# Performance work log

Measured on AMD Instinct MI355X. Metric: run time of the kernel, lower is better.

## Reference

```python
import jax, jax.numpy as jnp
import numpy as np

N_NODES = 50000
N_REL = 4
N_EDGES = 400000
IN_F, HID_F, OUT_F = 128, 128, 64


def _graphconv(h, s, d, W, b, n_nodes):
    """DGL GraphConv, norm='both': D_dst^{-1/2} A D_src^{-1/2} h W + b.
    Degrees clamped to min 1 (DGL behavior for isolated nodes)."""
    ones = jnp.ones(s.shape[0], h.dtype)
    deg_out = jnp.clip(jax.ops.segment_sum(ones, s, num_segments=n_nodes), 1.0)
    deg_in = jnp.clip(jax.ops.segment_sum(ones, d, num_segments=n_nodes), 1.0)
    # scale src features, transform first (weight applied pre-aggregation)
    hw = (h * jax.lax.rsqrt(deg_out)[:, None]) @ W          # [N, out]
    msg = hw[s]                                              # gather  [E, out]
    agg = jax.ops.segment_sum(msg, d, num_segments=n_nodes)  # scatter [N, out]
    return agg * jax.lax.rsqrt(deg_in)[:, None] + b


def _hetero_layer(h, src, dst, W, b):
    # HeteroGraphConv with aggregate='sum': sum per-relation GraphConv outputs
    n_nodes = h.shape[0]
    out = _graphconv(h, src[0], dst[0], W[0], b[0], n_nodes)
    for r in range(1, W.shape[0]):
        out = out + _graphconv(h, src[r], dst[r], W[r], b[r], n_nodes)
    return out


def setup_inputs() -> dict:
    key = jax.random.key(0)
    k = jax.random.split(key, 6)
    x = jax.random.normal(k[0], (N_NODES, IN_F), dtype=jnp.float32)
    src = jax.random.randint(k[1], (N_REL, N_EDGES), 0, N_NODES, dtype=jnp.int32)
    dst = jax.random.randint(k[2], (N_REL, N_EDGES), 0, N_NODES, dtype=jnp.int32)
    W1 = jax.random.normal(k[3], (N_REL, IN_F, HID_F), dtype=jnp.float32) / np.sqrt(IN_F)
    b1 = jnp.zeros((N_REL, HID_F), dtype=jnp.float32)
    W2 = jax.random.normal(k[4], (N_REL, HID_F, OUT_F), dtype=jnp.float32) / np.sqrt(HID_F)
    b2 = jnp.zeros((N_REL, OUT_F), dtype=jnp.float32)
    return {"x": x, "src": src, "dst": dst, "W1": W1, "b1": b1, "W2": W2, "b2": b2}


def reference(x, src, dst, W1, b1, W2, b2):
    h = _hetero_layer(x, src, dst, W1, b1)
    h = jax.nn.relu(h)
    return _hetero_layer(h, src, dst, W2, b2)
```

## Files before the change

### kernel.cpp

```cpp
#include <hip/hip_runtime.h>
#include <hip/hip_bf16.h>

#define N_NODES 50000
#define N_REL 4
#define N_EDGES 400000
#define CHUNK 1024
#define NCHUNK ((N_NODES + CHUNK - 1) / CHUNK)

#define EB 32
#define ECH (N_EDGES / EB)
#define NR 8
#define RNG (N_NODES / NR)

#define PX_BLOCKS 3125
#define PW_BLOCKS 192
#define HIST_BLOCKS (N_REL * EB * NR)

using short8 = __attribute__((ext_vector_type(8))) short;
using f32x4 = __attribute__((ext_vector_type(4))) float;

static __device__ inline unsigned short f2bf(float f) {
  unsigned u = __float_as_uint(f);
  unsigned r = (u + 0x7FFFu + ((u >> 16) & 1u)) >> 16;
  return (unsigned short)r;
}
static __device__ inline float bf2f(unsigned short b) {
  return __uint_as_float(((unsigned)b) << 16);
}
static __device__ inline void fma_bf2(unsigned w, float ds, float& a0,
                                      float& a1) {
  float lo = __uint_as_float(w << 16);
  float hi = __uint_as_float(w & 0xffff0000u);
  a0 = fmaf(lo, ds, a0);
  a1 = fmaf(hi, ds, a1);
}

__global__ __launch_bounds__(256) void k_prep_fused(
    const float* __restrict__ x, const float* __restrict__ W1,
    const float* __restrict__ W2, const int* __restrict__ src,
    const int* __restrict__ dst, unsigned short* __restrict__ xb,
    unsigned short* __restrict__ Wt1, unsigned short* __restrict__ Wt2,
    unsigned short* __restrict__ Hs, unsigned short* __restrict__ Hd,
    int* __restrict__ chunkSums) {
  __shared__ unsigned int ldsS[RNG / 2], ldsD[RNG / 2];
  const int b = blockIdx.x;
  const int tid = threadIdx.x;
  if (b < PX_BLOCKS) {
    if (b == 0 && tid < 64) chunkSums[tid] = 0;
    int i = b * 256 + tid;
    const float4* p = (const float4*)x + (size_t)i * 2;
    float4 v0 = p[0], v1 = p[1];
    unsigned short pk[8] = {f2bf(v0.x), f2bf(v0.y), f2bf(v0.z), f2bf(v0.w),
                            f2bf(v1.x), f2bf(v1.y), f2bf(v1.z), f2bf(v1.w)};
    *(uint4*)(xb + (size_t)i * 8) = *(uint4*)pk;
    return;
  }
  if (b < PX_BLOCKS + PW_BLOCKS) {
    int ob = (b - PX_BLOCKS) * 2 + (tid >> 7);
    int kk = tid & 127;
    if (ob < 128) {
      int c = ob;
#pragma unroll
      for (int r = 0; r < 4; ++r)
        Wt1[(size_t)c * 512 + r * 128 + kk] =
            f2bf(W1[(size_t)r * 16384 + kk * 128 + c]);
    } else {
      int c = ob - 128;
      int r = c >> 6, cc = c & 63;
      Wt2[(size_t)c * 128 + kk] = f2bf(W2[(size_t)r * 8192 + kk * 64 + cc]);
    }
    return;
  }
  const int hb = b - PX_BLOCKS - PW_BLOCKS;
  const int range = hb % NR;
  const int chunk = (hb / NR) % EB;
  const int rel = hb / (NR * EB);
  for (int i = tid; i < RNG / 2; i += 256) {
    ldsS[i] = 0u;
    ldsD[i] = 0u;
  }
  __syncthreads();
  const int n0 = range * RNG;
  const int* sp = src + (size_t)rel * N_EDGES + chunk * ECH;
  const int* dp = dst + (size_t)rel * N_EDGES + chunk * ECH;
  for (int e = tid; e < ECH; e += 256) {
    int s = sp[e] - n0;
    if ((unsigned)s < RNG) atomicAdd(&ldsS[s >> 1], 1u << ((s & 1) * 16));
    int d = dp[e] - n0;
    if ((unsigned)d < RNG) atomicAdd(&ldsD[d >> 1], 1u << ((d & 1) * 16));
  }
  __syncthreads();
  unsigned int* HsO =
      (unsigned int*)(Hs + ((size_t)rel * EB + chunk) * N_NODES + n0);
  unsigned int* HdO =
      (unsigned int*)(Hd + ((size_t)rel * EB + chunk) * N_NODES + n0);
  for (int i = tid; i < RNG / 2; i += 256) {
    HsO[i] = ldsS[i];
    HdO[i] = ldsD[i];
  }
}

__global__ __launch_bounds__(256) void k_reduce_m(
    const unsigned short* __restrict__ Hs, unsigned short* __restrict__ Hd,
    int* __restrict__ cnt_m, float* __restrict__ dso, float* __restrict__ dsi,
    ushort4* __restrict__ relOff, int* __restrict__ chunkSums) {
  int n = blockIdx.x * 256 + threadIdx.x;
  int run = 0;
  if (n < N_NODES) {
#pragma unroll
    for (int r = 0; r < N_REL; ++r) {
      int so = 0;
#pragma unroll
      for (int b = 0; b < EB; ++b)
        so += Hs[((size_t)r * EB + b) * N_NODES + n];
      dso[r * N_NODES + n] = rsqrtf((float)(so < 1 ? 1 : so));
    }
    unsigned short rs[4];
#pragma unroll
    for (int r = 0; r < N_REL; ++r) {
      rs[r] = (unsigned short)run;
#pragma unroll
      for (int b = 0; b < EB; ++b) {
        size_t off = ((size_t)r * EB + b) * N_NODES + n;
        int v = Hd[off];
        Hd[off] = (unsigned short)run;
        run += v;
      }
      int di = run - rs[r];
      dsi[r * N_NODES + n] = rsqrtf((float)(di < 1 ? 1 : di));
    }
    cnt_m[n] = run;
    relOff[n] = make_ushort4(rs[0], rs[1], rs[2], rs[3]);
  }
  __shared__ int red[256];
  red[threadIdx.x] = run;
  __syncthreads();
  for (int off = 128; off > 0; off >>= 1) {
    if (threadIdx.x < off) red[threadIdx.x] += red[threadIdx.x + off];
    __syncthreads();
  }
  if (threadIdx.x == 0) atomicAdd(&chunkSums[blockIdx.x >> 2], red[0]);
}

__global__ __launch_bounds__(64) void k_scan_chunks(int* __restrict__ chunkSums,
                                                    int* __restrict__ row_ptr) {
  if (threadIdx.x == 0) {
    int running = 0;
    for (int c = 0; c < NCHUNK; ++c) {
      int v = chunkSums[c];
      chunkSums[c] = running;
      running += v;
    }
    row_ptr[N_NODES] = N_REL * N_EDGES;
  }
}

__global__ __launch_bounds__(256) void k_scan_within(
    const int* __restrict__ cnt_m, const int* __restrict__ chunkOff,
    int* __restrict__ row_ptr) {
  int c = blockIdx.x;
  int t = threadIdx.x;
  int base = c * CHUNK + t * 4;
  int v[4];
#pragma unroll
  for (int j = 0; j < 4; ++j) {
    int n = base + j;
    v[j] = (n < N_NODES) ? cnt_m[n] : 0;
  }
  int total = v[0] + v[1] + v[2] + v[3];
  __shared__ int lds[256];
  lds[t] = total;
  __syncthreads();
  for (int off = 1; off < 256; off <<= 1) {
    int add = (t >= off) ? lds[t - off] : 0;
    __syncthreads();
    lds[t] += add;
    __syncthreads();
  }
  int thrExcl = lds[t] - total + chunkOff[c];
  int pre = 0;
#pragma unroll
  for (int j = 0; j < 4; ++j) {
    int n = base + j;
    if (n < N_NODES) row_ptr[n] = thrExcl + pre;
    pre += v[j];
  }
}

__global__ __launch_bounds__(256) void k_fill2m(
    const int* __restrict__ src, const int* __restrict__ dst,
    const unsigned short* __restrict__ Hd, const int* __restrict__ row_ptr,
    unsigned short* __restrict__ sorted) {
  const int range = blockIdx.x % NR;
  const int chunk = (blockIdx.x / NR) % EB;
  const int rel = blockIdx.x / (NR * EB);
  __shared__ unsigned int cur[RNG];
  const int n0 = range * RNG;
  const int* rp = row_ptr + n0;
  const unsigned short* pref = Hd + ((size_t)rel * EB + chunk) * N_NODES + n0;
  for (int i = threadIdx.x; i < RNG; i += 256)
    cur[i] = (unsigned)(rp[i] + pref[i]);
  __syncthreads();
  const int* sp = src + (size_t)rel * N_EDGES + chunk * ECH;
  const int* dp = dst + (size_t)rel * N_EDGES + chunk * ECH;
  for (int e = threadIdx.x; e < ECH; e += 256) {
    int d = dp[e] - n0;
    if ((unsigned)d < RNG) {
      unsigned pos = atomicAdd(&cur[d], 1u);
      sorted[pos] = (unsigned short)sp[e];
    }
  }
}

__global__ __launch_bounds__(256) void k_gather1a(
    const unsigned short* __restrict__ xb, const int* __restrict__ row_ptr,
    const ushort4* __restrict__ relOff, const unsigned short* __restrict__ sortedm,
    const float* __restrict__ dso, const float* __restrict__ dsi,
    unsigned int* __restrict__ agg) {
  const int wave = threadIdx.x >> 6, lane = threadIdx.x & 63;
  const int g = lane & 31;
  const int node = blockIdx.x * 8 + wave * 2 + (lane >> 5);
  const int rp = row_ptr[node], rp1 = row_ptr[node + 1];
  const ushort4 ro = relOff[node];
  const int beg[4] = {rp + ro.x, rp + ro.y, rp + ro.z, rp + ro.w};
  const int end4[4] = {rp + ro.y, rp + ro.z, rp + ro.w, rp1};
#pragma unroll
  for (int r = 0; r < 4; ++r) {
    const float* dsoR = dso + (size_t)r * N_NODES;
    float a0[4] = {0, 0, 0, 0}, a1[4] = {0, 0, 0, 0};
    float a2[4] = {0, 0, 0, 0}, a3[4] = {0, 0, 0, 0};
    for (int base = beg[r]; base < end4[r]; base += 32) {
      int n = end4[r] - base;
      if (n > 32) n = 32;
      int my = (g < n) ? (int)sortedm[base + g] : 0;
      int j = 0;
      for (; j + 3 < n; j += 4) {
#pragma unroll
        for (int k = 0; k < 4; ++k) {
          int s = __shfl(my, j + k, 32);
          float ds = dsoR[s];
          uint2 w = *(const uint2*)(xb + (size_t)s * 128 + g * 4);
          fma_bf2(w.x, ds, a0[k], a1[k]);
          fma_bf2(w.y, ds, a2[k], a3[k]);
        }
      }
      for (; j < n; ++j) {
        int s = __shfl(my, j, 32);
        float ds = dsoR[s];
        uint2 w = *(const uint2*)(xb + (size_t)s * 128 + g * 4);
        fma_bf2(w.x, ds, a0[0], a1[0]);
        fma_bf2(w.y, ds, a2[0], a3[0]);
      }
    }
    float di = dsi[(size_t)r * N_NODES + node];
    float t0 = ((a0[0] + a0[1]) + (a0[2] + a0[3])) * di;
    float t1 = ((a1[0] + a1[1]) + (a1[2] + a1[3])) * di;
    float t2 = ((a2[0] + a2[1]) + (a2[2] + a2[3])) * di;
    float t3 = ((a3[0] + a3[1]) + (a3[2] + a3[3])) * di;
    uint2 pk;
    pk.x = (unsigned)f2bf(t0) | ((unsigned)f2bf(t1) << 16);
    pk.y = (unsigned)f2bf(t2) | ((unsigned)f2bf(t3) << 16);
    *((uint2*)agg + ((size_t)node * 4 + r) * 32 + g) = pk;
  }
}

__global__ __launch_bounds__(256, 2) void k_gemm_h1(
    const unsigned short* __restrict__ agg, const unsigned short* __restrict__ Wt,
    const float* __restrict__ b1, unsigned short* __restrict__ h1, int M) {
  __shared__ unsigned short Alds[64 * 128];
  __shared__ unsigned short Wlds[128 * 128];
  const int tid = threadIdx.x;
  const int wid = tid >> 6, lane = tid & 63;
  const int rowBase = blockIdx.x * 64;
  const int lrow = lane & 15;
  const int quarter = lane >> 4;

  f32x4 acc[4][2];
#pragma unroll
  for (int i = 0; i < 4; ++i)
#pragma unroll
    for (int j = 0; j < 2; ++j) acc[i][j] = (f32x4){0.f, 0.f, 0.f, 0.f};

  for (int k0 = 0; k0 < 4; ++k0) {
    __syncthreads();
#pragma unroll
    for (int it = 0; it < 4; ++it) {
      int cid = tid + it * 256;
      int row = cid >> 4, kg = cid & 15;
      int grow = rowBase + row;
      uint4 v = make_uint4(0, 0, 0, 0);
      if (grow < M)
        v = *(const uint4*)(agg + (size_t)grow * 512 + k0 * 128 + kg * 8);
      *(uint4*)(Alds + row * 128 + ((kg ^ (row & 7)) * 8)) = v;
    }
#pragma unroll
    for (int it = 0; it < 8; ++it) {
      int cid = tid + it * 256;
      int c = cid >> 4, kg = cid & 15;
      uint4 v = *(const uint4*)(Wt + (size_t)c * 512 + k0 * 128 + kg * 8);
      *(uint4*)(Wlds + c * 128 + ((kg ^ (c & 7)) * 8)) = v;
    }
    __syncthreads();
#pragma unroll
    for (int kk = 0; kk < 4; ++kk) {
      int kg = kk * 4 + quarter;
      short8 a[4], b[2];
#pragma unroll
      for (int i = 0; i < 4; ++i) {
        int row = i * 16 + lrow;
        a[i] = *(const short8*)(Alds + row * 128 + ((kg ^ (row & 7)) * 8));
      }
#pragma unroll
      for (int j = 0; j < 2; ++j) {
        int c = wid * 32 + j * 16 + lrow;
        b[j] = *(const short8*)(Wlds + c * 128 + ((kg ^ (c & 7)) * 8));
      }
#pragma unroll
      for (int i = 0; i < 4; ++i)
#pragma unroll
        for (int j = 0; j < 2; ++j)
          acc[i][j] = __builtin_amdgcn_mfma_f32_16x16x32_bf16(a[i], b[j],
                                                              acc[i][j], 0, 0, 0);
    }
  }

#pragma unroll
  for (int j = 0; j < 2; ++j) {
    int c = wid * 32 + j * 16 + lrow;
    float bs = b1[c] + b1[128 + c] + b1[256 + c] + b1[384 + c];
#pragma unroll
    for (int i = 0; i < 4; ++i) {
#pragma unroll
      for (int r = 0; r < 4; ++r) {
        int grow = rowBase + i * 16 + quarter * 4 + r;
        if (grow < M)
          h1[(size_t)grow * 128 + c] = f2bf(fmaxf(acc[i][j][r] + bs, 0.f));
      }
    }
  }
}

template <int REL_COLS>
__global__ __launch_bounds__(256, 2) void k_gemm_mfma(
    const unsigned short* __restrict__ A, const unsigned short* __restrict__ Wt,
    const float* __restrict__ dsoBase, unsigned short* __restrict__ C,
    int cstride, int M) {
  __shared__ unsigned short Alds[64 * 128];
  __shared__ unsigned short Wlds[256 * 128];
  const int tid = threadIdx.x;
  const int wid = tid >> 6, lane = tid & 63;
  const int rowBase = blockIdx.x * 64;

#pragma unroll
  for (int i = 0; i < 4; ++i) {
    int cid = tid + i * 256;
    int row = cid >> 4, kg = cid & 15;
    int grow = rowBase + row;
    uint4 v = make_uint4(0, 0, 0, 0);
    if (grow < M) v = *(const uint4*)(A + (size_t)grow * 128 + kg * 8);
    *(uint4*)(Alds + row * 128 + ((kg ^ (row & 7)) * 8)) = v;
  }
#pragma unroll
  for (int i = 0; i < 16; ++i) {
    int cid = tid + i * 256;
    int row = cid >> 4, kg = cid & 15;
    uint4 v = *(const uint4*)(Wt + (size_t)row * 128 + kg * 8);
    *(uint4*)(Wlds + row * 128 + ((kg ^ (row & 7)) * 8)) = v;
  }
  __syncthreads();

  f32x4 acc[4][4];
#pragma unroll
  for (int i = 0; i < 4; ++i)
#pragma unroll
    for (int j = 0; j < 4; ++j) acc[i][j] = (f32x4){0.f, 0.f, 0.f, 0.f};

  const int lrow = lane & 15;
  const int khalf = lane >> 4;
#pragma unroll
  for (int k0 = 0; k0 < 4; ++k0) {
    int kg = k0 * 4 + khalf;
    short8 a[4], b[4];
#pragma unroll
    for (int i = 0; i < 4; ++i) {
      int row = i * 16 + lrow;
      a[i] = *(const short8*)(Alds + row * 128 + ((kg ^ (row & 7)) * 8));
    }
#pragma unroll
    for (int j = 0; j < 4; ++j) {
      int wrow = wid * 64 + j * 16 + lrow;
      b[j] = *(const short8*)(Wlds + wrow * 128 + ((kg ^ (wrow & 7)) * 8));
    }
#pragma unroll
    for (int i = 0; i < 4; ++i)
#pragma unroll
      for (int j = 0; j < 4; ++j)
        acc[i][j] = __builtin_amdgcn_mfma_f32_16x16x32_bf16(a[i], b[j],
                                                            acc[i][j], 0, 0, 0);
  }

#pragma unroll
  for (int i = 0; i < 4; ++i) {
#pragma unroll
    for (int j = 0; j < 4; ++j) {
      int col = wid * 64 + j * 16 + (lane & 15);
      const float* dsoCol = dsoBase + (size_t)(col / REL_COLS) * N_NODES;
#pragma unroll
      for (int r = 0; r < 4; ++r) {
        int grow = rowBase + i * 16 + (lane >> 4) * 4 + r;
        if (grow < M)
          C[(size_t)grow * cstride + col] = f2bf(acc[i][j][r] * dsoCol[grow]);
      }
    }
  }
}

__global__ __launch_bounds__(256) void k_gather2m(
    const unsigned short* __restrict__ Y, const int* __restrict__ row_ptr,
    const ushort4* __restrict__ relOff, const unsigned short* __restrict__ sortedm,
    const float* __restrict__ dsi, const float* __restrict__ b2,
    float* __restrict__ out) {
  const int wave = threadIdx.x >> 6, lane = threadIdx.x & 63;
  const int g = lane & 15;
  const int node = blockIdx.x * 16 + wave * 4 + (lane >> 4);
  const int rp = row_ptr[node], rp1 = row_ptr[node + 1];
  const ushort4 ro = relOff[node];
  const int beg[4] = {rp + ro.x, rp + ro.y, rp + ro.z, rp + ro.w};
  const int end4[4] = {rp + ro.y, rp + ro.z, rp + ro.w, rp1};
  float t0 = 0.f, t1 = 0.f, t2 = 0.f, t3 = 0.f;
#pragma unroll
  for (int r = 0; r < 4; ++r) {
    float a0[4] = {0, 0, 0, 0}, a1[4] = {0, 0, 0, 0};
    float a2[4] = {0, 0, 0, 0}, a3[4] = {0, 0, 0, 0};
    for (int base = beg[r]; base < end4[r]; base += 16) {
      int n = end4[r] - base;
      if (n > 16) n = 16;
      int my = (g < n) ? (int)sortedm[base + g] : 0;
      int j = 0;
      for (; j + 3 < n; j += 4) {
#pragma unroll
        for (int k = 0; k < 4; ++k) {
          int s = __shfl(my, j + k, 16);
          uint2 w = *(const uint2*)(Y + ((size_t)s * 4 + r) * 64 + g * 4);
          fma_bf2(w.x, 1.f, a0[k], a1[k]);
          fma_bf2(w.y, 1.f, a2[k], a3[k]);
        }
      }
      for (; j < n; ++j) {
        int s = __shfl(my, j, 16);
        uint2 w = *(const uint2*)(Y + ((size_t)s * 4 + r) * 64 + g * 4);
        fma_bf2(w.x, 1.f, a0[0], a1[0]);
        fma_bf2(w.y, 1.f, a2[0], a3[0]);
      }
    }
    float di = dsi[(size_t)r * N_NODES + node];
    t0 = fmaf((a0[0] + a0[1]) + (a0[2] + a0[3]), di, t0);
    t1 = fmaf((a1[0] + a1[1]) + (a1[2] + a1[3]), di, t1);
    t2 = fmaf((a2[0] + a2[1]) + (a2[2] + a2[3]), di, t2);
    t3 = fmaf((a3[0] + a3[1]) + (a3[2] + a3[3]), di, t3);
  }
#pragma unroll
  for (int r = 0; r < 4; ++r) {
    float4 bb = *(const float4*)(b2 + r * 64 + g * 4);
    t0 += bb.x;
    t1 += bb.y;
    t2 += bb.z;
    t3 += bb.w;
  }
  *(float4*)(out + (size_t)node * 64 + g * 4) = make_float4(t0, t1, t2, t3);
}

extern "C" void kernel_launch(void* const* d_in, const int* in_sizes, int n_in,
                              void* d_out, int out_size, void* d_ws,
                              size_t ws_size, hipStream_t stream) {
  const float* x  = (const float*)d_in[0];
  const int* src  = (const int*)d_in[1];
  const int* dst  = (const int*)d_in[2];
  const float* W1 = (const float*)d_in[3];
  const float* b1 = (const float*)d_in[4];
  const float* W2 = (const float*)d_in[5];
  const float* b2 = (const float*)d_in[6];
  float* out = (float*)d_out;

  char* wsb = (char*)d_ws;
  unsigned short* Hs = (unsigned short*)wsb;
  unsigned short* h1 = (unsigned short*)wsb;
  unsigned short* Hd = Hs + (size_t)N_REL * EB * N_NODES;
  unsigned short* xb = Hd + (size_t)N_REL * EB * N_NODES;
  unsigned short* agg = xb + (size_t)N_NODES * 128;
  unsigned short* Y2 = agg;
  char* tail = (char*)(agg + (size_t)N_NODES * 512);
  unsigned short* Wt1 = (unsigned short*)tail;
  unsigned short* Wt2 = Wt1 + 128 * 512;
  float* dso = (float*)(Wt2 + 256 * 128);
  float* dsi = dso + N_REL * N_NODES;
  ushort4* relOff = (ushort4*)(dsi + N_REL * N_NODES);
  int* cnt_m = (int*)(relOff + N_NODES);
  int* row_ptr = cnt_m + N_NODES;
  int* chunkSums = row_ptr + (N_NODES + 1);
  unsigned short* sorted = (unsigned short*)(chunkSums + 64);

  k_prep_fused<<<PX_BLOCKS + PW_BLOCKS + HIST_BLOCKS, 256, 0, stream>>>(
      x, W1, W2, src, dst, xb, Wt1, Wt2, Hs, Hd, chunkSums);
  k_reduce_m<<<(N_NODES + 255) / 256, 256, 0, stream>>>(Hs, Hd, cnt_m, dso,
                                                        dsi, relOff, chunkSums);
  k_scan_chunks<<<1, 64, 0, stream>>>(chunkSums, row_ptr);
  k_scan_within<<<NCHUNK, 256, 0, stream>>>(cnt_m, chunkSums, row_ptr);
  k_fill2m<<<N_REL * EB * NR, 256, 0, stream>>>(src, dst, Hd, row_ptr, sorted);

  k_gather1a<<<N_NODES / 8, 256, 0, stream>>>(xb, row_ptr, relOff, sorted, dso,
                                              dsi, (unsigned int*)agg);
  k_gemm_h1<<<(N_NODES + 63) / 64, 256, 0, stream>>>(agg, Wt1, b1, h1,
                                                     N_NODES);
  k_gemm_mfma<64><<<(N_NODES + 63) / 64, 256, 0, stream>>>(h1, Wt2, dso, Y2,
                                                           256, N_NODES);
  k_gather2m<<<N_NODES / 16, 256, 0, stream>>>(Y2, row_ptr, relOff, sorted,
                                               dsi, b2, out);
}
```

Measured before the change: 267.1 us.

## Fuse layer-1 gather with its GEMM through an LDS tile, halve histogram ranges

The layer-1 neighbour gather and the following bf16 MFMA GEMM become one kernel. Each block aggregates 32 nodes across the four relations into a padded LDS tile, then multiplies that tile by W1 with the weights read straight from global memory. This removes the global write and re-read of the 50000x512 aggregation buffer and one launch. In exchange each block does its gather and its GEMM back to back with no overlap, and weights are fetched from global memory per wave instead of staged in LDS. NR also drops from 8 to 4, which halves the histogram/fill blocks but makes each block cover a larger node range.

```diff
diff --git a/kernel.cpp b/kernel.cpp
--- a/kernel.cpp
+++ b/kernel.cpp
@@ -9,12 +9,14 @@
 
 #define EB 32
 #define ECH (N_EDGES / EB)
-#define NR 8
+#define NR 4
 #define RNG (N_NODES / NR)
 
 #define PX_BLOCKS 3125
 #define PW_BLOCKS 192
 #define HIST_BLOCKS (N_REL * EB * NR)
+
+#define AST 520
 
 using short8 = __attribute__((ext_vector_type(8))) short;
 using f32x4 = __attribute__((ext_vector_type(4))) float;
@@ -212,129 +214,102 @@
   }
 }
 
-__global__ __launch_bounds__(256) void k_gather1a(
+__global__ __launch_bounds__(256, 3) void k_fused_l1(
     const unsigned short* __restrict__ xb, const int* __restrict__ row_ptr,
     const ushort4* __restrict__ relOff, const unsigned short* __restrict__ sortedm,
     const float* __restrict__ dso, const float* __restrict__ dsi,
-    unsigned int* __restrict__ agg) {
+    const unsigned short* __restrict__ Wt, const float* __restrict__ b1,
+    unsigned short* __restrict__ h1) {
+  __shared__ unsigned short Atile[32 * AST];
   const int wave = threadIdx.x >> 6, lane = threadIdx.x & 63;
   const int g = lane & 31;
-  const int node = blockIdx.x * 8 + wave * 2 + (lane >> 5);
-  const int rp = row_ptr[node], rp1 = row_ptr[node + 1];
-  const ushort4 ro = relOff[node];
-  const int beg[4] = {rp + ro.x, rp + ro.y, rp + ro.z, rp + ro.w};
-  const int end4[4] = {rp + ro.y, rp + ro.z, rp + ro.w, rp1};
-#pragma unroll
-  for (int r = 0; r < 4; ++r) {
-    const float* dsoR = dso + (size_t)r * N_NODES;
-    float a0[4] = {0, 0, 0, 0}, a1[4] = {0, 0, 0, 0};
-    float a2[4] = {0, 0, 0, 0}, a3[4] = {0, 0, 0, 0};
-    for (int base = beg[r]; base < end4[r]; base += 32) {
-      int n = end4[r] - base;
-      if (n > 32) n = 32;
-      int my = (g < n) ? (int)sortedm[base + g] : 0;
-      int j = 0;
-      for (; j + 3 < n; j += 4) {
-#pragma unroll
-        for (int k = 0; k < 4; ++k) {
-          int s = __shfl(my, j + k, 32);
-          float ds = dsoR[s];
-          uint2 w = *(const uint2*)(xb + (size_t)s * 128 + g * 4);
-          fma_bf2(w.x, ds, a0[k], a1[k]);
-          fma_bf2(w.y, ds, a2[k], a3[k]);
+  const int nodeBase = blockIdx.x * 32;
+
+  for (int p = 0; p < 4; ++p) {
+    const int local = p * 8 + wave * 2 + (lane >> 5);
+    const int node = nodeBase + local;
+    if (node < N_NODES) {
+      const int rp = row_ptr[node], rp1 = row_ptr[node + 1];
+      const ushort4 ro = relOff[node];
+      const int beg[4] = {rp + ro.x, rp + ro.y, rp + ro.z, rp + ro.w};
+      const int end4[4] = {rp + ro.y, rp + ro.z, rp + ro.w, rp1};
+#pragma unroll
+      for (int r = 0; r < 4; ++r) {
+        const float* dsoR = dso + (size_t)r * N_NODES;
+        float a0[4] = {0, 0, 0, 0}, a1[4] = {0, 0, 0, 0};
+        float a2[4] = {0, 0, 0, 0}, a3[4] = {0, 0, 0, 0};
+        for (int base = beg[r]; base < end4[r]; base += 32) {
+          int n = end4[r] - base;
+          if (n > 32) n = 32;
+          int my = (g < n) ? (int)sortedm[base + g] : 0;
+          int j = 0;
+          for (; j + 3 < n; j += 4) {
+#pragma unroll
+            for (int k = 0; k < 4; ++k) {
+              int s = __shfl(my, j + k, 32);
+              float ds = dsoR[s];
+              uint2 w = *(const uint2*)(xb + (size_t)s * 128 + g * 4);
+              fma_bf2(w.x, ds, a0[k], a1[k]);
+              fma_bf2(w.y, ds, a2[k], a3[k]);
+            }
+          }
+          for (; j < n; ++j) {
+            int s = __shfl(my, j, 32);
+            float ds = dsoR[s];
+            uint2 w = *(const uint2*)(xb + (size_t)s * 128 + g * 4);
+            fma_bf2(w.x, ds, a0[0], a1[0]);
+            fma_bf2(w.y, ds, a2[0], a3[0]);
+          }
         }
-      }
-      for (; j < n; ++j) {
-        int s = __shfl(my, j, 32);
-        float ds = dsoR[s];
-        uint2 w = *(const uint2*)(xb + (size_t)s * 128 + g * 4);
-        fma_bf2(w.x, ds, a0[0], a1[0]);
-        fma_bf2(w.y, ds, a2[0], a3[0]);
-      }
-    }
-    float di = dsi[(size_t)r * N_NODES + node];
-    float t0 = ((a0[0] + a0[1]) + (a0[2] + a0[3])) * di;
-    float t1 = ((a1[0] + a1[1]) + (a1[2] + a1[3])) * di;
-    float t2 = ((a2[0] + a2[1]) + (a2[2] + a2[3])) * di;
-    float t3 = ((a3[0] + a3[1]) + (a3[2] + a3[3])) * di;
-    uint2 pk;
-    pk.x = (unsigned)f2bf(t0) | ((unsigned)f2bf(t1) << 16);
-    pk.y = (unsigned)f2bf(t2) | ((unsigned)f2bf(t3) << 16);
-    *((uint2*)agg + ((size_t)node * 4 + r) * 32 + g) = pk;
-  }
-}
-
-__global__ __launch_bounds__(256, 2) void k_gemm_h1(
-    const unsigned short* __restrict__ agg, const unsigned short* __restrict__ Wt,
-    const float* __restrict__ b1, unsigned short* __restrict__ h1, int M) {
-  __shared__ unsigned short Alds[64 * 128];
-  __shared__ unsigned short Wlds[128 * 128];
-  const int tid = threadIdx.x;
-  const int wid = tid >> 6, lane = tid & 63;
-  const int rowBase = blockIdx.x * 64;
-  const int lrow = lane & 15;
-  const int quarter = lane >> 4;
-
-  f32x4 acc[4][2];
-#pragma unroll
-  for (int i = 0; i < 4; ++i)
+        float di = dsi[(size_t)r * N_NODES + node];
+        float t0 = ((a0[0] + a0[1]) + (a0[2] + a0[3])) * di;
+        float t1 = ((a1[0] + a1[1]) + (a1[2] + a1[3])) * di;
+        float t2 = ((a2[0] + a2[1]) + (a2[2] + a2[3])) * di;
+        float t3 = ((a3[0] + a3[1]) + (a3[2] + a3[3])) * di;
+        uint2 pk;
+        pk.x = (unsigned)f2bf(t0) | ((unsigned)f2bf(t1) << 16);
+        pk.y = (unsigned)f2bf(t2) | ((unsigned)f2bf(t3) << 16);
+        *((uint2*)(Atile + local * AST + r * 128 + g * 4)) = pk;
+      }
+    } else {
+      uint2 z = make_uint2(0u, 0u);
+#pragma unroll
+      for (int r = 0; r < 4; ++r)
+        *((uint2*)(Atile + local * AST + r * 128 + g * 4)) = z;
+    }
+  }
+  __syncthreads();
+
+  const int lrow = lane & 15, quarter = lane >> 4;
+  f32x4 acc[2][2];
+#pragma unroll
+  for (int i = 0; i < 2; ++i)
 #pragma unroll
     for (int j = 0; j < 2; ++j) acc[i][j] = (f32x4){0.f, 0.f, 0.f, 0.f};
-
-  for (int k0 = 0; k0 < 4; ++k0) {
-    __syncthreads();
-#pragma unroll
-    for (int it = 0; it < 4; ++it) {
-      int cid = tid + it * 256;
-      int row = cid >> 4, kg = cid & 15;
-      int grow = rowBase + row;
-      uint4 v = make_uint4(0, 0, 0, 0);
-      if (grow < M)
-        v = *(const uint4*)(agg + (size_t)grow * 512 + k0 * 128 + kg * 8);
-      *(uint4*)(Alds + row * 128 + ((kg ^ (row & 7)) * 8)) = v;
-    }
-#pragma unroll
-    for (int it = 0; it < 8; ++it) {
-      int cid = tid + it * 256;
-      int c = cid >> 4, kg = cid & 15;
-      uint4 v = *(const uint4*)(Wt + (size_t)c * 512 + k0 * 128 + kg * 8);
-      *(uint4*)(Wlds + c * 128 + ((kg ^ (c & 7)) * 8)) = v;
-    }
-    __syncthreads();
-#pragma unroll
-    for (int kk = 0; kk < 4; ++kk) {
-      int kg = kk * 4 + quarter;
-      short8 a[4], b[2];
-#pragma unroll
-      for (int i = 0; i < 4; ++i) {
-        int row = i * 16 + lrow;
-        a[i] = *(const short8*)(Alds + row * 128 + ((kg ^ (row & 7)) * 8));
-      }
-#pragma unroll
-      for (int j = 0; j < 2; ++j) {
-        int c = wid * 32 + j * 16 + lrow;
-        b[j] = *(const short8*)(Wlds + c * 128 + ((kg ^ (c & 7)) * 8));
-      }
-#pragma unroll
-      for (int i = 0; i < 4; ++i)
-#pragma unroll
-        for (int j = 0; j < 2; ++j)
-          acc[i][j] = __builtin_amdgcn_mfma_f32_16x16x32_bf16(a[i], b[j],
-                                                              acc[i][j], 0, 0, 0);
-    }
-  }
-
+  const unsigned short* WtW = Wt + (size_t)(wave * 32) * 512;
+#pragma unroll 4
+  for (int kk = 0; kk < 16; ++kk) {
+    int kg = kk * 4 + quarter;
+    short8 a0 = *(const short8*)(Atile + (0 * 16 + lrow) * AST + kg * 8);
+    short8 a1 = *(const short8*)(Atile + (1 * 16 + lrow) * AST + kg * 8);
+    short8 b0 = *(const short8*)(WtW + (size_t)(0 * 16 + lrow) * 512 + kg * 8);
+    short8 b1v = *(const short8*)(WtW + (size_t)(1 * 16 + lrow) * 512 + kg * 8);
+    acc[0][0] = __builtin_amdgcn_mfma_f32_16x16x32_bf16(a0, b0, acc[0][0], 0, 0, 0);
+    acc[0][1] = __builtin_amdgcn_mfma_f32_16x16x32_bf16(a0, b1v, acc[0][1], 0, 0, 0);
+    acc[1][0] = __builtin_amdgcn_mfma_f32_16x16x32_bf16(a1, b0, acc[1][0], 0, 0, 0);
+    acc[1][1] = __builtin_amdgcn_mfma_f32_16x16x32_bf16(a1, b1v, acc[1][1], 0, 0, 0);
+  }
 #pragma unroll
   for (int j = 0; j < 2; ++j) {
-    int c = wid * 32 + j * 16 + lrow;
+    int c = wave * 32 + j * 16 + lrow;
     float bs = b1[c] + b1[128 + c] + b1[256 + c] + b1[384 + c];
 #pragma unroll
-    for (int i = 0; i < 4; ++i) {
-#pragma unroll
-      for (int r = 0; r < 4; ++r) {
-        int grow = rowBase + i * 16 + quarter * 4 + r;
-        if (grow < M)
-          h1[(size_t)grow * 128 + c] = f2bf(fmaxf(acc[i][j][r] + bs, 0.f));
+    for (int i = 0; i < 2; ++i) {
+#pragma unroll
+      for (int rr = 0; rr < 4; ++rr) {
+        int grow = nodeBase + i * 16 + quarter * 4 + rr;
+        if (grow < N_NODES)
+          h1[(size_t)grow * 128 + c] = f2bf(fmaxf(acc[i][j][rr] + bs, 0.f));
       }
     }
   }
@@ -487,9 +462,8 @@
   unsigned short* h1 = (unsigned short*)wsb;
   unsigned short* Hd = Hs + (size_t)N_REL * EB * N_NODES;
   unsigned short* xb = Hd + (size_t)N_REL * EB * N_NODES;
-  unsigned short* agg = xb + (size_t)N_NODES * 128;
-  unsigned short* Y2 = agg;
-  char* tail = (char*)(agg + (size_t)N_NODES * 512);
+  unsigned short* Y2 = xb + (size_t)N_NODES * 128;
+  char* tail = (char*)(Y2 + (size_t)N_NODES * 256);
   unsigned short* Wt1 = (unsigned short*)tail;
   unsigned short* Wt2 = Wt1 + 128 * 512;
   float* dso = (float*)(Wt2 + 256 * 128);
@@ -508,10 +482,8 @@
   k_scan_within<<<NCHUNK, 256, 0, stream>>>(cnt_m, chunkSums, row_ptr);
   k_fill2m<<<N_REL * EB * NR, 256, 0, stream>>>(src, dst, Hd, row_ptr, sorted);
 
-  k_gather1a<<<N_NODES / 8, 256, 0, stream>>>(xb, row_ptr, relOff, sorted, dso,
-                                              dsi, (unsigned int*)agg);
-  k_gemm_h1<<<(N_NODES + 63) / 64, 256, 0, stream>>>(agg, Wt1, b1, h1,
-                                                     N_NODES);
+  k_fused_l1<<<(N_NODES + 31) / 32, 256, 0, stream>>>(
+      xb, row_ptr, relOff, sorted, dso, dsi, Wt1, b1, h1);
   k_gemm_mfma<64><<<(N_NODES + 63) / 64, 256, 0, stream>>>(h1, Wt2, dso, Y2,
                                                            256, N_NODES);
   k_gather2m<<<N_NODES / 16, 256, 0, stream>>>(Y2, row_ptr, relOff, sorted,
```

New measurement: 294.1 us. 10.1% more time.
